# Kernel tuning notes

Hardware: AMD Instinct MI355X
Metric: run time of the kernel (lower is better)

The kernel has to match this reference:

```python
import jax, jax.numpy as jnp
import numpy as np

B, D, G = 64, 1024, 64  # batch, features==units (required by the source einsum), num_groups


def setup_inputs() -> dict:
    key = jax.random.key(0)
    ks = jax.random.split(key, 8)
    return {
        "x": jax.random.normal(ks[0], (B, D), jnp.float32),
        "gid": jax.random.randint(ks[1], (B,), 0, G, dtype=jnp.int32),
        # mean-field variational parameters per group (weights flattened to D*D as in the source)
        "w_mu": jax.random.normal(ks[2], (G, D * D), jnp.float32) * 0.05,
        "w_sigma": jax.random.normal(ks[3], (G, D * D), jnp.float32) * 0.1 - 3.0,  # raw scale params
        "b_mu": jnp.zeros((G, D), jnp.float32),
        "b_sigma": jax.random.normal(ks[4], (G, D), jnp.float32) * 0.1 - 3.0,
        # reparameterization noise (explicit so forward is deterministic)
        "eps_w": jax.random.normal(ks[5], (B, D * D), jnp.float32),
        "eps_b": jax.random.normal(ks[6], (B, D), jnp.float32),
    }


def reference(x, gid, w_mu, w_sigma, b_mu, b_sigma, eps_w, eps_b):
    # Gather group-specific posterior params and sample via reparameterization.
    # scale = softplus(raw) matches the standard tfp mean-field parameterization.
    w_samp = w_mu[gid] + jax.nn.softplus(w_sigma[gid]) * eps_w  # (B, D*D)
    b_samp = b_mu[gid] + jax.nn.softplus(b_sigma[gid]) * eps_b  # (B, D)
    # Reshape((-1, units)): (B, num_features, units) = (B, D, D)
    w = w_samp.reshape(B, D, D)
    # tf.einsum('Bup,Bp->Bu', w, x): per-sample matmul (axis1 labeled u, axis2 labeled p)
    out = jnp.einsum("bup,bp->bu", w, x) + b_samp  # (B, D)
    return jax.nn.relu(out)
```

## Files before the change

### kernel.cpp

```cpp
#include <hip/hip_runtime.h>
#include <math.h>

#define BB 64
#define DD 1024
#define GG 64

__device__ __forceinline__ float softplus_fast(float z) {
    const float LOG2E = 1.44269504088896340736f;
    const float LN2   = 0.69314718055994530942f;
    float t = __builtin_amdgcn_exp2f(-LOG2E * fabsf(z));
    float l = __builtin_amdgcn_logf(1.0f + t);
    return fmaxf(z, 0.0f) + LN2 * l;
}

__global__ __launch_bounds__(256) void mld_kernel(
    const float* __restrict__ x, const int* __restrict__ gid,
    const float* __restrict__ w_mu, const float* __restrict__ w_sigma,
    const float* __restrict__ b_mu, const float* __restrict__ b_sigma,
    const float* __restrict__ eps_w, const float* __restrict__ eps_b,
    float* __restrict__ out)
{
    const int wave = (int)((blockIdx.x * blockDim.x + threadIdx.x) >> 6);
    const int lane = (int)(threadIdx.x & 63);
    const int b = wave >> 10;
    const int u = wave & 1023;
    const int g = gid[b];

    const float4* __restrict__ xr  = (const float4*)(x + (size_t)b * DD);
    const float4* __restrict__ wmr = (const float4*)(w_mu    + ((size_t)g * DD + u) * DD);
    const float4* __restrict__ wsr = (const float4*)(w_sigma + ((size_t)g * DD + u) * DD);
    const float4* __restrict__ ewr = (const float4*)(eps_w   + ((size_t)b * DD + u) * DD);

    float acc = 0.0f;
    #pragma unroll
    for (int k = 0; k < 4; ++k) {
        const int i = lane + k * 64;
        const float4 xm = xr[i];
        const float4 wm = wmr[i];
        const float4 ws = wsr[i];
        const float4 ew = ewr[i];
        acc += (wm.x + softplus_fast(ws.x) * ew.x) * xm.x;
        acc += (wm.y + softplus_fast(ws.y) * ew.y) * xm.y;
        acc += (wm.z + softplus_fast(ws.z) * ew.z) * xm.z;
        acc += (wm.w + softplus_fast(ws.w) * ew.w) * xm.w;
    }

    #pragma unroll
    for (int off = 32; off > 0; off >>= 1)
        acc += __shfl_down(acc, off, 64);

    if (lane == 0) {
        const size_t gu = (size_t)g * DD + u;
        const size_t bu = (size_t)b * DD + u;
        const float bs = b_mu[gu] + softplus_fast(b_sigma[gu]) * eps_b[bu];
        const float o = acc + bs;
        out[bu] = fmaxf(o, 0.0f);
    }
}

extern "C" void kernel_launch(void* const* d_in, const int* in_sizes, int n_in,
                              void* d_out, int out_size, void* d_ws, size_t ws_size,
                              hipStream_t stream) {
    const float* x       = (const float*)d_in[0];
    const int*   gid     = (const int*)d_in[1];
    const float* w_mu    = (const float*)d_in[2];
    const float* w_sigma = (const float*)d_in[3];
    const float* b_mu    = (const float*)d_in[4];
    const float* b_sigma = (const float*)d_in[5];
    const float* eps_w   = (const float*)d_in[6];
    const float* eps_b   = (const float*)d_in[7];
    float* out = (float*)d_out;

    const int total_waves = BB * DD;
    const int blocks = total_waves / 4;
    mld_kernel<<<blocks, 256, 0, stream>>>(x, gid, w_mu, w_sigma, b_mu, b_sigma,
                                           eps_w, eps_b, out);
}
```

Measured before the change: 116.0 us.

## Process four output rows per wave and swizzle block order across XCDs

```diff
diff --git a/kernel.cpp b/kernel.cpp
--- a/kernel.cpp
+++ b/kernel.cpp
@@ -4,6 +4,12 @@
 #define BB 64
 #define DD 1024
 #define GG 64
+#define F4 (DD / 4)
+#define ROWS 4
+#define WAVES_PB 4
+#define U_PER_BLOCK (ROWS * WAVES_PB)
+#define BLOCKS_PER_B (DD / U_PER_BLOCK)
+#define NWG (BB * BLOCKS_PER_B)
 
 __device__ __forceinline__ float softplus_fast(float z) {
     const float LOG2E = 1.44269504088896340736f;
@@ -20,40 +26,56 @@
     const float* __restrict__ eps_w, const float* __restrict__ eps_b,
     float* __restrict__ out)
 {
-    const int wave = (int)((blockIdx.x * blockDim.x + threadIdx.x) >> 6);
     const int lane = (int)(threadIdx.x & 63);
-    const int b = wave >> 10;
-    const int u = wave & 1023;
-    const int g = gid[b];
+    const int wid  = (int)(threadIdx.x >> 6);
+
+    const int bid     = (int)blockIdx.x;
+    const int logical = (bid & 7) * (NWG >> 3) + (bid >> 3);
+
+    const int b    = logical >> 6;
+    const int ublk = logical & 63;
+    const int u0   = ublk * U_PER_BLOCK + wid * ROWS;
+    const int g    = gid[b];
 
     const float4* __restrict__ xr  = (const float4*)(x + (size_t)b * DD);
-    const float4* __restrict__ wmr = (const float4*)(w_mu    + ((size_t)g * DD + u) * DD);
-    const float4* __restrict__ wsr = (const float4*)(w_sigma + ((size_t)g * DD + u) * DD);
-    const float4* __restrict__ ewr = (const float4*)(eps_w   + ((size_t)b * DD + u) * DD);
+    const float4* __restrict__ wmr = (const float4*)(w_mu    + ((size_t)g * DD + u0) * DD);
+    const float4* __restrict__ wsr = (const float4*)(w_sigma + ((size_t)g * DD + u0) * DD);
+    const float4* __restrict__ ewr = (const float4*)(eps_w   + ((size_t)b * DD + u0) * DD);
 
-    float acc = 0.0f;
+    float acc[ROWS] = {0.f, 0.f, 0.f, 0.f};
+
     #pragma unroll
     for (int k = 0; k < 4; ++k) {
         const int i = lane + k * 64;
         const float4 xm = xr[i];
-        const float4 wm = wmr[i];
-        const float4 ws = wsr[i];
-        const float4 ew = ewr[i];
-        acc += (wm.x + softplus_fast(ws.x) * ew.x) * xm.x;
-        acc += (wm.y + softplus_fast(ws.y) * ew.y) * xm.y;
-        acc += (wm.z + softplus_fast(ws.z) * ew.z) * xm.z;
-        acc += (wm.w + softplus_fast(ws.w) * ew.w) * xm.w;
+        #pragma unroll
+        for (int r = 0; r < ROWS; ++r) {
+            const int j = r * F4 + i;
+            const float4 wm = wmr[j];
+            const float4 ws = wsr[j];
+            const float4 ew = ewr[j];
+            float a = acc[r];
+            a += (wm.x + softplus_fast(ws.x) * ew.x) * xm.x;
+            a += (wm.y + softplus_fast(ws.y) * ew.y) * xm.y;
+            a += (wm.z + softplus_fast(ws.z) * ew.z) * xm.z;
+            a += (wm.w + softplus_fast(ws.w) * ew.w) * xm.w;
+            acc[r] = a;
+        }
     }
 
     #pragma unroll
-    for (int off = 32; off > 0; off >>= 1)
-        acc += __shfl_down(acc, off, 64);
+    for (int off = 32; off > 0; off >>= 1) {
+        #pragma unroll
+        for (int r = 0; r < ROWS; ++r)
+            acc[r] += __shfl_xor(acc[r], off, 64);
+    }
 
-    if (lane == 0) {
+    if (lane < ROWS) {
+        const int u = u0 + lane;
         const size_t gu = (size_t)g * DD + u;
         const size_t bu = (size_t)b * DD + u;
         const float bs = b_mu[gu] + softplus_fast(b_sigma[gu]) * eps_b[bu];
-        const float o = acc + bs;
+        const float o = acc[lane] + bs;
         out[bu] = fmaxf(o, 0.0f);
     }
 }
@@ -71,8 +93,6 @@
     const float* eps_b   = (const float*)d_in[7];
     float* out = (float*)d_out;
 
-    const int total_waves = BB * DD;
-    const int blocks = total_waves / 4;
-    mld_kernel<<<blocks, 256, 0, stream>>>(x, gid, w_mu, w_sigma, b_mu, b_sigma,
-                                           eps_w, eps_b, out);
+    mld_kernel<<<NWG, 256, 0, stream>>>(x, gid, w_mu, w_sigma, b_mu, b_sigma,
+                                        eps_w, eps_b, out);
 }
```

Measured after the change: 125.2 us. 1.08x slower.
